# Performance work log

Hardware: AMD Instinct MI355X
Metric: run time of the kernel (lower is better)

The kernel has to match this reference:

```python
import jax, jax.numpy as jnp
import numpy as np

EMBED_DIM = 1024
HEAD_DIM = 64


def setup_inputs() -> dict:
    key = jax.random.key(0)
    ks = jax.random.split(key, 9)
    B, S, E, H = 4, 2048, EMBED_DIM, HEAD_DIM
    s = 1.0 / np.sqrt(E)
    return {
        "query": jax.random.normal(ks[0], (B, S, E), dtype=jnp.float32),
        "key": jax.random.normal(ks[1], (B, S, E), dtype=jnp.float32),
        "value": jax.random.normal(ks[2], (B, S, E), dtype=jnp.float32),
        "Wq": jax.random.normal(ks[3], (E, H), dtype=jnp.float32) * s,
        "bq": jnp.zeros((H,), dtype=jnp.float32),
        "Wk": jax.random.normal(ks[4], (E, H), dtype=jnp.float32) * s,
        "bk": jnp.zeros((H,), dtype=jnp.float32),
        "Wv": jax.random.normal(ks[5], (E, H), dtype=jnp.float32) * s,
        "bv": jnp.zeros((H,), dtype=jnp.float32),
    }


def reference(query, key, value, Wq, bq, Wk, bk, Wv, bv):
    # per-head linear projections: [B,S,E] @ [E,H] -> [B,S,H]
    q = jnp.einsum("bse,eh->bsh", query, Wq) + bq
    k = jnp.einsum("bse,eh->bsh", key, Wk) + bk
    v = jnp.einsum("bse,eh->bsh", value, Wv) + bv
    # NOTE: original code computes dim_k but never scales -> unscaled scores
    scores = jnp.einsum("bqh,bkh->bqk", q, k)  # [B,S,S]
    weights = jax.nn.softmax(scores, axis=-1)
    return jnp.einsum("bqk,bkh->bqh", weights, v)  # [B,S,H]
```

## Files before the change

### kernel.cpp

```cpp
#include <hip/hip_runtime.h>
#include <math.h>

#define B 4
#define S 2048
#define E 1024
#define H 64
#define BS (B*S)
#define LOG2E 1.44269504088896f
#define CINIT (-69.2493662f)

typedef float v4f __attribute__((ext_vector_type(4)));
typedef short v8s __attribute__((ext_vector_type(8)));
typedef unsigned short u16;
typedef u16 u16x8 __attribute__((ext_vector_type(8)));
typedef u16 u16x4 __attribute__((ext_vector_type(4)));

#define MFMA(a,b,c) __builtin_amdgcn_mfma_f32_16x16x32_bf16(a,b,c,0,0,0)

__device__ inline u16 rh_bf16(float x){ return (u16)((__float_as_uint(x)+0x8000u)>>16); }

__global__ __launch_bounds__(256) void wsetup_kernel(
    const float* __restrict__ Wq, const float* __restrict__ Wk,
    const float* __restrict__ Wv,
    u16* __restrict__ Wt_hi, u16* __restrict__ Wt_lo)
{
    __shared__ float wt[64][65];
    const int t  = threadIdx.x;
    const int p  = blockIdx.x >> 4;
    const int e0 = (blockIdx.x & 15) * 64;
    const float* Wsrc = (p==0) ? Wq : (p==1 ? Wk : Wv);
    const float scale = (p==0) ? LOG2E : 1.0f;

    #pragma unroll
    for (int i=0;i<16;i++){
        int e_l = i*4 + (t>>6);
        wt[e_l][t&63] = Wsrc[(size_t)(e0+e_l)*H + (t&63)] * scale;
    }
    __syncthreads();

    const int h = t>>2, e16 = (t&3)*16;
    u16 hi_a[16], lo_a[16];
    #pragma unroll
    for (int j=0;j<16;j++){
        float f = wt[e16+j][h];
        unsigned u = __float_as_uint(f);
        hi_a[j] = (u16)(u>>16);
        float hif = __uint_as_float(u & 0xFFFF0000u);
        lo_a[j] = rh_bf16(f - hif);
    }
    u16* dh = Wt_hi + (size_t)(p*64+h)*E + e0 + e16;
    u16* dl = Wt_lo + (size_t)(p*64+h)*E + e0 + e16;
    *(u16x8*)dh     = *(u16x8*)&hi_a[0];
    *(u16x8*)(dh+8) = *(u16x8*)&hi_a[8];
    *(u16x8*)dl     = *(u16x8*)&lo_a[0];
    *(u16x8*)(dl+8) = *(u16x8*)&lo_a[8];
}

__global__ __launch_bounds__(128) void proj_kernel(
    const float* __restrict__ query, const float* __restrict__ key_,
    const float* __restrict__ value,
    const u16* __restrict__ Wt_hi, const u16* __restrict__ Wt_lo,
    const float* __restrict__ bq, const float* __restrict__ bk,
    const float* __restrict__ bv,
    u16* __restrict__ q_hi, u16* __restrict__ q_lo,
    u16* __restrict__ k_hi, u16* __restrict__ k_lo,
    u16* __restrict__ vt)
{
    __shared__ __align__(16) u16 xh[32][136], xl[32][136];
    __shared__ __align__(16) u16 wh[64][136], wl[64][136];

    const int t  = threadIdx.x;
    const int p  = blockIdx.x >> 8;
    const int r0 = (blockIdx.x & 255) * 32;
    const float* xp = (p==0) ? query : (p==1 ? key_ : value);
    const int wv = t>>6, lane = t&63, m = lane&15, quad = lane>>4;

    const int srow = t>>2, se16 = (t&3)*16;
    const int swh  = t>>1, seo  = (t&1)*64;

    v4f acc[4];
    #pragma unroll
    for (int nt=0;nt<4;nt++) acc[nt] = (v4f){0.f,0.f,0.f,0.f};

    for (int ec=0; ec<8; ec++){
        const int e0 = ec*128;
        __syncthreads();
        #pragma unroll
        for (int half=0; half<2; half++){
            const int col = half*64 + se16;
            const float* xr = xp + (size_t)(r0+srow)*E + e0 + col;
            float4 aa[4];
            aa[0] = *(const float4*)(xr);
            aa[1] = *(const float4*)(xr+4);
            aa[2] = *(const float4*)(xr+8);
            aa[3] = *(const float4*)(xr+12);
            float fv[16];
            #pragma unroll
            for (int q4=0;q4<4;q4++){
                fv[q4*4+0]=aa[q4].x; fv[q4*4+1]=aa[q4].y;
                fv[q4*4+2]=aa[q4].z; fv[q4*4+3]=aa[q4].w;
            }
            u16 ha[16], la[16];
            #pragma unroll
            for (int j=0;j<16;j++){
                unsigned u = __float_as_uint(fv[j]);
                ha[j] = (u16)(u>>16);
                la[j] = rh_bf16(fv[j] - __uint_as_float(u & 0xFFFF0000u));
            }
            *(u16x8*)&xh[srow][col]   = *(u16x8*)&ha[0];
            *(u16x8*)&xh[srow][col+8] = *(u16x8*)&ha[8];
            *(u16x8*)&xl[srow][col]   = *(u16x8*)&la[0];
            *(u16x8*)&xl[srow][col+8] = *(u16x8*)&la[8];
        }
        {
            const u16* sh = Wt_hi + (size_t)(p*64+swh)*E + e0 + seo;
            const u16* sl = Wt_lo + (size_t)(p*64+swh)*E + e0 + seo;
            #pragma unroll
            for (int i=0;i<8;i++){
                *(u16x8*)&wh[swh][seo + i*8] = *(const u16x8*)(sh + i*8);
                *(u16x8*)&wl[swh][seo + i*8] = *(const u16x8*)(sl + i*8);
            }
        }
        __syncthreads();

        v8s ah[4], al[4];
        #pragma unroll
        for (int c=0;c<4;c++){
            ah[c] = *(v8s*)&xh[wv*16+m][c*32 + quad*8];
            al[c] = *(v8s*)&xl[wv*16+m][c*32 + quad*8];
        }
        #pragma unroll
        for (int nt=0;nt<4;nt++){
            v4f d = acc[nt];
            #pragma unroll
            for (int c=0;c<4;c++){
                v8s bh = *(v8s*)&wh[nt*16+m][c*32 + quad*8];
                v8s bl = *(v8s*)&wl[nt*16+m][c*32 + quad*8];
                d = MFMA(ah[c], bh, d);
                d = MFMA(al[c], bh, d);
                d = MFMA(ah[c], bl, d);
            }
            acc[nt] = d;
        }
    }

    const float* bp = (p==0) ? bq : (p==1 ? bk : bv);
    const float bscale = (p==0) ? LOG2E : 1.0f;
    #pragma unroll
    for (int nt=0;nt<4;nt++){
        const int hl = nt*16+m;
        const float bb = bp[hl]*bscale;
        #pragma unroll
        for (int r=0;r<4;r++){
            const int gr = r0 + wv*16 + quad*4 + r;
            const float val = acc[nt][r] + bb;
            if (p<2){
                unsigned u = __float_as_uint(val);
                u16 hi = (u16)(u>>16);
                float hif = __uint_as_float(u & 0xFFFF0000u);
                u16 lo = rh_bf16(val - hif);
                u16* dh = (p==0) ? q_hi : k_hi;
                u16* dl = (p==0) ? q_lo : k_lo;
                dh[(size_t)gr*H + hl] = hi;
                dl[(size_t)gr*H + hl] = lo;
            } else {
                const int vb_ = gr >> 11;
                const int vs  = gr & 2047;
                vt[((size_t)(vb_*H) + hl)*S + vs] = rh_bf16(val);
            }
        }
    }
}

__global__ __launch_bounds__(256) void attn_kernel(
    const u16* __restrict__ qh_g, const u16* __restrict__ ql_g,
    const u16* __restrict__ kh_g, const u16* __restrict__ kl_g,
    const u16* __restrict__ vt_g,
    float* __restrict__ accw, float* __restrict__ lw, int ksplit)
{
    __shared__ __align__(16) u16 khe[4][16][72];
    __shared__ __align__(16) u16 kle[4][16][72];
    __shared__ __align__(16) u16 vtl[64][72];
    __shared__ __align__(16) u16 pl[4][16][72];

    const int t = threadIdx.x;
    const int wv = t>>6, lane = t&63, m = lane&15, quad = lane>>4;
    const int bid = blockIdx.x;
    const int qb = bid / ksplit, chunk = bid % ksplit;
    const int b = qb >> 5, s0 = (qb & 31)*64;
    const int ck = S / ksplit;
    const int j0base = chunk * ck;
    const int iters = ck / 64;

    const u16* qr  = qh_g + (size_t)(b*S + s0 + wv*16 + m)*H + quad*8;
    const u16* qrl = ql_g + (size_t)(b*S + s0 + wv*16 + m)*H + quad*8;
    const v8s qh0 = *(const v8s*)(qr),  qh1 = *(const v8s*)(qr+32);
    const v8s ql0 = *(const v8s*)(qrl), ql1 = *(const v8s*)(qrl+32);

    v4f oacc[4];
    #pragma unroll
    for (int nt=0;nt<4;nt++) oacc[nt] = (v4f){0.f,0.f,0.f,0.f};
    float lp[4] = {0.f,0.f,0.f,0.f};
    const v4f cinit = (v4f){CINIT,CINIT,CINIT,CINIT};

    const int sj = t>>2, sh16 = (t&3)*16;
    const u16* khs = kh_g + (size_t)(b*S + j0base + sj)*H + sh16;
    const u16* kls = kl_g + (size_t)(b*S + j0base + sj)*H + sh16;
    u16* khd = &khe[sj&3][sj>>2][sh16];
    u16* kld = &kle[sj&3][sj>>2][sh16];
    const int vh = t>>2, vj16 = (t&3)*16;
    const u16* vts = vt_g + (size_t)(b*H + vh)*S + j0base + vj16;
    u16* vtd = &vtl[vh][vj16];

    for (int it=0; it<iters; ++it){
        __syncthreads();
        {
            const u16* s1 = khs + (size_t)it*64*H;
            const u16* s2 = kls + (size_t)it*64*H;
            const u16* s3 = vts + it*64;
            *(u16x8*)(khd)   = *(const u16x8*)(s1);
            *(u16x8*)(khd+8) = *(const u16x8*)(s1+8);
            *(u16x8*)(kld)   = *(const u16x8*)(s2);
            *(u16x8*)(kld+8) = *(const u16x8*)(s2+8);
            *(u16x8*)(vtd)   = *(const u16x8*)(s3);
            *(u16x8*)(vtd+8) = *(const u16x8*)(s3+8);
        }
        __syncthreads();

        v4f sc[4];
        #pragma unroll
        for (int jt=0;jt<4;jt++){
            const u16* kr  = &khe[jt][m][quad*8];
            const u16* krl = &kle[jt][m][quad*8];
            v8s b0 = *(const v8s*)kr,  b1 = *(const v8s*)(kr+32);
            v8s c0 = *(const v8s*)krl, c1 = *(const v8s*)(krl+32);
            v4f d = cinit;
            d = MFMA(qh0,b0,d); d = MFMA(qh1,b1,d);
            d = MFMA(ql0,b0,d); d = MFMA(ql1,b1,d);
            d = MFMA(qh0,c0,d); d = MFMA(qh1,c1,d);
            sc[jt] = d;
        }

        #pragma unroll
        for (int r=0;r<4;r++){
            float p0 = exp2f(sc[0][r]);
            float p1 = exp2f(sc[1][r]);
            float p2 = exp2f(sc[2][r]);
            float p3 = exp2f(sc[3][r]);
            lp[r] += (p0 + p1) + (p2 + p3);
            u16x4 pk;
            pk[0] = rh_bf16(p0); pk[1] = rh_bf16(p1);
            pk[2] = rh_bf16(p2); pk[3] = rh_bf16(p3);
            *(u16x4*)&pl[wv][quad*4+r][4*m] = pk;
        }

        #pragma unroll
        for (int c=0;c<2;c++){
            v8s pa = *(const v8s*)&pl[wv][m][c*32 + quad*8];
            #pragma unroll
            for (int nt=0;nt<4;nt++){
                v8s vb = *(const v8s*)&vtl[nt*16+m][c*32 + quad*8];
                oacc[nt] = MFMA(pa, vb, oacc[nt]);
            }
        }
    }

    #pragma unroll
    for (int r=0;r<4;r++){
        float v = lp[r];
        v += __shfl_xor(v,1); v += __shfl_xor(v,2);
        v += __shfl_xor(v,4); v += __shfl_xor(v,8);
        lp[r] = v;
    }
    const int growb = b*S + s0 + wv*16;
    if (m==0){
        float4 lv; lv.x=lp[0]; lv.y=lp[1]; lv.z=lp[2]; lv.w=lp[3];
        *(float4*)(lw + (size_t)chunk*BS + growb + quad*4) = lv;
    }
    float* ab = accw + ((size_t)chunk*BS + growb)*H;
    #pragma unroll
    for (int nt=0;nt<4;nt++){
        #pragma unroll
        for (int r=0;r<4;r++)
            ab[(size_t)(quad*4+r)*H + nt*16 + m] = oacc[nt][r];
    }
}

__global__ __launch_bounds__(256) void merge_kernel(
    const float* __restrict__ accw, const float* __restrict__ lw,
    float* __restrict__ out, int ksplit)
{
    const int idx = blockIdx.x*256 + threadIdx.x;
    const int row = idx >> 4, h4 = (idx & 15)*4;
    float4 a = {0.f,0.f,0.f,0.f};
    float ls = 0.f;
    for (int c=0;c<ksplit;c++){
        const float4 t4 = *(const float4*)(accw + ((size_t)c*BS + row)*H + h4);
        a.x+=t4.x; a.y+=t4.y; a.z+=t4.z; a.w+=t4.w;
        ls += lw[(size_t)c*BS + row];
    }
    const float inv = __builtin_amdgcn_rcpf(ls);
    float4 o; o.x=a.x*inv; o.y=a.y*inv; o.z=a.z*inv; o.w=a.w*inv;
    *(float4*)(out + (size_t)row*H + h4) = o;
}

extern "C" void kernel_launch(void* const* d_in, const int* in_sizes, int n_in,
                              void* d_out, int out_size, void* d_ws, size_t ws_size,
                              hipStream_t stream) {
    const float* query = (const float*)d_in[0];
    const float* key_  = (const float*)d_in[1];
    const float* value = (const float*)d_in[2];
    const float* Wq    = (const float*)d_in[3];
    const float* bq    = (const float*)d_in[4];
    const float* Wk    = (const float*)d_in[5];
    const float* bk    = (const float*)d_in[6];
    const float* Wv    = (const float*)d_in[7];
    const float* bv    = (const float*)d_in[8];
    float* out = (float*)d_out;

    char* base = (char*)d_ws;
    size_t off = 0;
    u16* Wt_hi = (u16*)(base + off); off += (size_t)3*64*E*2;
    u16* Wt_lo = (u16*)(base + off); off += (size_t)3*64*E*2;
    u16* q_hi  = (u16*)(base + off); off += (size_t)BS*H*2;
    u16* q_lo  = (u16*)(base + off); off += (size_t)BS*H*2;
    u16* k_hi  = (u16*)(base + off); off += (size_t)BS*H*2;
    u16* k_lo  = (u16*)(base + off); off += (size_t)BS*H*2;
    u16* v_bf  = (u16*)(base + off); off += (size_t)BS*H*2;
    u16* vt    = (u16*)(base + off); off += (size_t)BS*H*2;
    (void)v_bf;
    const size_t fixed = off;
    const size_t CH = (size_t)BS*H*4 + (size_t)BS*4;

    int K = 1;
    if      (ws_size >= fixed + 8*CH) K = 8;
    else if (ws_size >= fixed + 4*CH) K = 4;
    else if (ws_size >= fixed + 2*CH) K = 2;

    float* lw   = (float*)(base + fixed);
    float* accw = (float*)(base + fixed + (size_t)K*BS*4);

    wsetup_kernel<<<48, 256, 0, stream>>>(Wq, Wk, Wv, Wt_hi, Wt_lo);
    proj_kernel<<<768, 128, 0, stream>>>(query, key_, value, Wt_hi, Wt_lo,
                                         bq, bk, bv, q_hi, q_lo, k_hi, k_lo, vt);
    attn_kernel<<<128*K, 256, 0, stream>>>(q_hi, q_lo, k_hi, k_lo, vt, accw, lw, K);
    merge_kernel<<<512, 256, 0, stream>>>(accw, lw, out, K);
}
```

Baseline: 182.3 us.

## Rewrite projection kernel to load operands directly into MFMA registers without LDS

The projection kernel drops its shared-memory staging and __syncthreads barriers. Each single-wave block now handles 16 rows, reading fp32 inputs and the bf16 hi/lo weights straight from global memory in MFMA fragment layout, with twice as many blocks launched. This removes LDS traffic and barrier stalls and raises block-level parallelism. In exchange, weights are re-read from global memory or L2 per 16-row block instead of being shared across 32 rows, and the strided per-lane loads are less coalesced.

```diff
diff --git a/kernel.cpp b/kernel.cpp
--- a/kernel.cpp
+++ b/kernel.cpp
@@ -18,6 +18,15 @@
 #define MFMA(a,b,c) __builtin_amdgcn_mfma_f32_16x16x32_bf16(a,b,c,0,0,0)
 
 __device__ inline u16 rh_bf16(float x){ return (u16)((__float_as_uint(x)+0x8000u)>>16); }
+
+__device__ inline void split8(const float4 a, const float4 b, v8s& hi, v8s& lo){
+    const float f0=a.x, f1=a.y, f2=a.z, f3=a.w, f4=b.x, f5=b.y, f6=b.z, f7=b.w;
+#define SP(i,val) { const unsigned u=__float_as_uint(val); \
+                    hi[i]=(short)(u>>16); \
+                    lo[i]=(short)rh_bf16((val)-__uint_as_float(u&0xFFFF0000u)); }
+    SP(0,f0) SP(1,f1) SP(2,f2) SP(3,f3) SP(4,f4) SP(5,f5) SP(6,f6) SP(7,f7)
+#undef SP
+}
 
 __global__ __launch_bounds__(256) void wsetup_kernel(
     const float* __restrict__ Wq, const float* __restrict__ Wk,
@@ -56,7 +65,7 @@
     *(u16x8*)(dl+8) = *(u16x8*)&lo_a[8];
 }
 
-__global__ __launch_bounds__(128) void proj_kernel(
+__global__ __launch_bounds__(64) void proj_kernel(
     const float* __restrict__ query, const float* __restrict__ key_,
     const float* __restrict__ value,
     const u16* __restrict__ Wt_hi, const u16* __restrict__ Wt_lo,
@@ -66,80 +75,34 @@
     u16* __restrict__ k_hi, u16* __restrict__ k_lo,
     u16* __restrict__ vt)
 {
-    __shared__ __align__(16) u16 xh[32][136], xl[32][136];
-    __shared__ __align__(16) u16 wh[64][136], wl[64][136];
-
-    const int t  = threadIdx.x;
-    const int p  = blockIdx.x >> 8;
-    const int r0 = (blockIdx.x & 255) * 32;
+    const int t = threadIdx.x;
+    const int m = t & 15, quad = t >> 4;
+    const int p  = blockIdx.x / 512;
+    const int r0 = (blockIdx.x % 512) * 16;
     const float* xp = (p==0) ? query : (p==1 ? key_ : value);
-    const int wv = t>>6, lane = t&63, m = lane&15, quad = lane>>4;
-
-    const int srow = t>>2, se16 = (t&3)*16;
-    const int swh  = t>>1, seo  = (t&1)*64;
+
+    const float* xrow = xp + (size_t)(r0+m)*E + quad*8;
+    const u16* wbh = Wt_hi + (size_t)(p*64+m)*E + quad*8;
+    const u16* wbl = Wt_lo + (size_t)(p*64+m)*E + quad*8;
 
     v4f acc[4];
-    #pragma unroll
-    for (int nt=0;nt<4;nt++) acc[nt] = (v4f){0.f,0.f,0.f,0.f};
-
-    for (int ec=0; ec<8; ec++){
-        const int e0 = ec*128;
-        __syncthreads();
-        #pragma unroll
-        for (int half=0; half<2; half++){
-            const int col = half*64 + se16;
-            const float* xr = xp + (size_t)(r0+srow)*E + e0 + col;
-            float4 aa[4];
-            aa[0] = *(const float4*)(xr);
-            aa[1] = *(const float4*)(xr+4);
-            aa[2] = *(const float4*)(xr+8);
-            aa[3] = *(const float4*)(xr+12);
-            float fv[16];
-            #pragma unroll
-            for (int q4=0;q4<4;q4++){
-                fv[q4*4+0]=aa[q4].x; fv[q4*4+1]=aa[q4].y;
-                fv[q4*4+2]=aa[q4].z; fv[q4*4+3]=aa[q4].w;
-            }
-            u16 ha[16], la[16];
-            #pragma unroll
-            for (int j=0;j<16;j++){
-                unsigned u = __float_as_uint(fv[j]);
-                ha[j] = (u16)(u>>16);
-                la[j] = rh_bf16(fv[j] - __uint_as_float(u & 0xFFFF0000u));
-            }
-            *(u16x8*)&xh[srow][col]   = *(u16x8*)&ha[0];
-            *(u16x8*)&xh[srow][col+8] = *(u16x8*)&ha[8];
-            *(u16x8*)&xl[srow][col]   = *(u16x8*)&la[0];
-            *(u16x8*)&xl[srow][col+8] = *(u16x8*)&la[8];
-        }
-        {
-            const u16* sh = Wt_hi + (size_t)(p*64+swh)*E + e0 + seo;
-            const u16* sl = Wt_lo + (size_t)(p*64+swh)*E + e0 + seo;
-            #pragma unroll
-            for (int i=0;i<8;i++){
-                *(u16x8*)&wh[swh][seo + i*8] = *(const u16x8*)(sh + i*8);
-                *(u16x8*)&wl[swh][seo + i*8] = *(const u16x8*)(sl + i*8);
-            }
-        }
-        __syncthreads();
-
-        v8s ah[4], al[4];
-        #pragma unroll
-        for (int c=0;c<4;c++){
-            ah[c] = *(v8s*)&xh[wv*16+m][c*32 + quad*8];
-            al[c] = *(v8s*)&xl[wv*16+m][c*32 + quad*8];
-        }
+    acc[0] = (v4f){0.f,0.f,0.f,0.f}; acc[1] = (v4f){0.f,0.f,0.f,0.f};
+    acc[2] = (v4f){0.f,0.f,0.f,0.f}; acc[3] = (v4f){0.f,0.f,0.f,0.f};
+
+    for (int it=0; it<32; ++it){
+        const int e0 = it*32;
+        const float4 xa = *(const float4*)(xrow + e0);
+        const float4 xb = *(const float4*)(xrow + e0 + 4);
+        v8s ah, al;
+        split8(xa, xb, ah, al);
         #pragma unroll
         for (int nt=0;nt<4;nt++){
+            const v8s bh = *(const v8s*)(wbh + (size_t)(nt*16)*E + e0);
+            const v8s bl = *(const v8s*)(wbl + (size_t)(nt*16)*E + e0);
             v4f d = acc[nt];
-            #pragma unroll
-            for (int c=0;c<4;c++){
-                v8s bh = *(v8s*)&wh[nt*16+m][c*32 + quad*8];
-                v8s bl = *(v8s*)&wl[nt*16+m][c*32 + quad*8];
-                d = MFMA(ah[c], bh, d);
-                d = MFMA(al[c], bh, d);
-                d = MFMA(ah[c], bl, d);
-            }
+            d = MFMA(ah, bh, d);
+            d = MFMA(al, bh, d);
+            d = MFMA(ah, bl, d);
             acc[nt] = d;
         }
     }
@@ -152,7 +115,7 @@
         const float bb = bp[hl]*bscale;
         #pragma unroll
         for (int r=0;r<4;r++){
-            const int gr = r0 + wv*16 + quad*4 + r;
+            const int gr = r0 + quad*4 + r;
             const float val = acc[nt][r] + bb;
             if (p<2){
                 unsigned u = __float_as_uint(val);
@@ -341,7 +304,7 @@
     float* accw = (float*)(base + fixed + (size_t)K*BS*4);
 
     wsetup_kernel<<<48, 256, 0, stream>>>(Wq, Wk, Wv, Wt_hi, Wt_lo);
-    proj_kernel<<<768, 128, 0, stream>>>(query, key_, value, Wt_hi, Wt_lo,
+    proj_kernel<<<1536, 64, 0, stream>>>(query, key_, value, Wt_hi, Wt_lo,
                                          bq, bk, bv, q_hi, q_lo, k_hi, k_lo, vt);
     attn_kernel<<<128*K, 256, 0, stream>>>(q_hi, q_lo, k_hi, k_lo, vt, accw, lw, K);
     merge_kernel<<<512, 256, 0, stream>>>(accw, lw, out, K);
```

New measurement: 212.0 us. +16.3%, slower.
